# Optimization experiments

Hardware: AMD Instinct MI355X
Metric: run time of the kernel (lower is better)

Reference implementation:

```python
import jax, jax.numpy as jnp
import numpy as np

NUM_HEADS = 32
HEAD_DIM = 128  # 4096 / 32


def setup_inputs() -> dict:
    key = jax.random.key(0)
    k1, k2, k3 = jax.random.split(key, 3)
    B, S, H = 1, 2048, 4096
    hidden_states = jax.random.normal(k1, (B, S, H), dtype=jnp.float32)
    # causal additive mask, broadcast over heads: 0 on/below diagonal, large negative above
    neg = jnp.finfo(jnp.float32).min
    causal = jnp.triu(jnp.full((S, S), neg, dtype=jnp.float32), k=1)
    attention_mask = causal[None, None, :, :]  # [1,1,S,S]
    w_pack = jax.random.normal(k2, (3 * H, H), dtype=jnp.float32) * 0.02
    w_o = jax.random.normal(k3, (H, H), dtype=jnp.float32) * 0.02
    return {"hidden_states": hidden_states, "attention_mask": attention_mask,
            "w_pack": w_pack, "w_o": w_o}


def reference(hidden_states, attention_mask, w_pack, w_o):
    B, S, H = hidden_states.shape
    nh, hd = NUM_HEADS, HEAD_DIM
    # fused QKV projection (Linear, no bias): x @ W^T
    proj = hidden_states @ w_pack.T                      # [B,S,3H]
    q, k, v = jnp.split(proj, 3, axis=-1)
    q = q.reshape(B, S, nh, hd).transpose(0, 2, 1, 3)    # [B,nh,S,hd]
    k = k.reshape(B, S, nh, hd).transpose(0, 2, 1, 3)
    v = v.reshape(B, S, nh, hd).transpose(0, 2, 1, 3)
    scale = 1.0 / jnp.sqrt(jnp.float32(hd))
    attn = jnp.einsum('bhqd,bhkd->bhqk', q, k) * scale   # [B,nh,S,S]
    attn = attn + attention_mask
    attn = jnp.maximum(attn, jnp.finfo(attn.dtype).min)  # clamp like torch.max(..., finfo.min)
    attn = jax.nn.softmax(attn, axis=-1)
    out = jnp.einsum('bhqk,bhkd->bhqd', attn, v)         # [B,nh,S,hd]
    out = out.transpose(0, 2, 1, 3).reshape(B, S, nh * hd)
    return out @ w_o.T                                    # [B,S,H]
```

## Files before the change

kernel.cpp:

```cpp
#include <hip/hip_runtime.h>
#include <stdint.h>

typedef __attribute__((ext_vector_type(8))) short short8;
typedef __attribute__((ext_vector_type(4))) float floatx4;

#define SEQ    2048
#define HID    4096
#define NHEAD  32
#define HDIMV  128
#define PROJN  12288

__device__ __forceinline__ unsigned short f2bf(float f) {
  union { float f; unsigned u; } v; v.f = f;
  unsigned r = (v.u + 0x7fffu + ((v.u >> 16) & 1u)) >> 16;
  return (unsigned short)r;
}

__device__ __forceinline__ void g2l16(const void* g, void* l) {
  __builtin_amdgcn_global_load_lds(
      (const __attribute__((address_space(1))) void*)g,
      (__attribute__((address_space(3))) void*)l, 16, 0, 0);
}

__global__ __launch_bounds__(256) void pack_fp32(const float* __restrict__ src,
                                                 unsigned short* __restrict__ dst, int K,
                                                 int scale_rows, float scale) {
  const int rp = blockIdx.x, kt = blockIdx.y, t = threadIdx.x;
  const long tb = ((long)rp * gridDim.y + kt) * 8192;
#pragma unroll
  for (int j = 0; j < 4; j++) {
    int ch = t + j * 256;
    int r = ch & 127, cc = ch >> 7;
    float sc = (rp * 128 + r < scale_rows) ? scale : 1.0f;
    const float* s = src + (long)(rp * 128 + r) * K + kt * 64 + cc * 8;
    float4 a = *(const float4*)s;
    float4 b = *(const float4*)(s + 4);
    short8 o;
    o[0] = (short)f2bf(a.x * sc); o[1] = (short)f2bf(a.y * sc);
    o[2] = (short)f2bf(a.z * sc); o[3] = (short)f2bf(a.w * sc);
    o[4] = (short)f2bf(b.x * sc); o[5] = (short)f2bf(b.y * sc);
    o[6] = (short)f2bf(b.z * sc); o[7] = (short)f2bf(b.w * sc);
    *(short8*)(dst + tb + ch * 8) = o;
  }
}

template<int OUT_F32>
__global__ __launch_bounds__(256, 4) void gemm_pk(
    const unsigned short* __restrict__ Ap,
    const unsigned short* __restrict__ Bp,
    void* __restrict__ C, int N, int K) {
  __shared__ __align__(16) unsigned short As[8192];
  __shared__ __align__(16) unsigned short Bs[8192];
  const int t = threadIdx.x;
  const int wave = t >> 6, lane = t & 63;
  const int bid = blockIdx.x;
  const int xcd = bid & 7;
  const int li = bid >> 3;
  const int mi = li & 15;
  const int ni = (li >> 4) * 8 + xcd;
  const int KT = K >> 6;
  const unsigned short* at = Ap + (long)mi * KT * 8192 + t * 8;
  const unsigned short* bt = Bp + (long)ni * KT * 8192 + t * 8;
  unsigned short* asl = As + wave * 512;
  unsigned short* bsl = Bs + wave * 512;

  const int mw = (wave >> 1) * 64;
  const int nw = (wave & 1) * 64;
  const int lq = lane & 15, lg = lane >> 4;

  floatx4 zero = {0.f, 0.f, 0.f, 0.f};
  floatx4 acc[4][4];
  for (int i = 0; i < 4; i++)
    for (int j = 0; j < 4; j++) acc[i][j] = zero;

  for (int kt = 0; kt < KT; kt++) {
    __syncthreads();
    const unsigned short* ak = at + (long)kt * 8192;
    const unsigned short* bk = bt + (long)kt * 8192;
#pragma unroll
    for (int j = 0; j < 4; j++) g2l16(ak + j * 2048, asl + j * 2048);
#pragma unroll
    for (int j = 0; j < 4; j++) g2l16(bk + j * 2048, bsl + j * 2048);
    __syncthreads();
#pragma unroll
    for (int kk = 0; kk < 2; kk++) {
      const int ch = (kk * 4 + lg) * 1024;
      short8 af[4], bfr[4];
#pragma unroll
      for (int i = 0; i < 4; i++)
        af[i] = *(const short8*)(As + ch + (mw + i * 16 + lq) * 8);
#pragma unroll
      for (int j = 0; j < 4; j++)
        bfr[j] = *(const short8*)(Bs + ch + (nw + j * 16 + lq) * 8);
#pragma unroll
      for (int i = 0; i < 4; i++)
#pragma unroll
        for (int j = 0; j < 4; j++)
          acc[i][j] = __builtin_amdgcn_mfma_f32_16x16x32_bf16(af[i], bfr[j], acc[i][j], 0, 0, 0);
    }
  }

  const int row0 = mi * 128 + mw + lg * 4;
  const int col0 = ni * 128 + nw + lq;
  if (OUT_F32) {
    float* Cf = (float*)C;
#pragma unroll
    for (int i = 0; i < 4; i++)
#pragma unroll
      for (int j = 0; j < 4; j++)
#pragma unroll
        for (int r = 0; r < 4; r++)
          Cf[(long)(row0 + i * 16 + r) * N + col0 + j * 16] = acc[i][j][r];
  } else {
    unsigned short* Cb = (unsigned short*)C;
#pragma unroll
    for (int i = 0; i < 4; i++)
#pragma unroll
      for (int j = 0; j < 4; j++)
#pragma unroll
        for (int r = 0; r < 4; r++)
          Cb[(long)(row0 + i * 16 + r) * N + col0 + j * 16] = f2bf(acc[i][j][r]);
  }
}

__global__ __launch_bounds__(256, 4) void gemm_qkv(
    const unsigned short* __restrict__ Ap,
    const unsigned short* __restrict__ Bp,
    unsigned short* __restrict__ Qf,
    unsigned short* __restrict__ Kf,
    unsigned short* __restrict__ Vf) {
  __shared__ __align__(16) unsigned short As[8192];
  __shared__ __align__(16) unsigned short Bs[8192];
  const int t = threadIdx.x;
  const int wave = t >> 6, lane = t & 63;
  const int bid = blockIdx.x;
  const int xcd = bid & 7;
  const int li = bid >> 3;
  const int mi = li & 15;
  const int ni = (li >> 4) * 8 + xcd;
  const int KT = HID >> 6;
  const unsigned short* at = Ap + (long)mi * KT * 8192 + t * 8;
  const unsigned short* bt = Bp + (long)ni * KT * 8192 + t * 8;
  unsigned short* asl = As + wave * 512;
  unsigned short* bsl = Bs + wave * 512;

  const int mw = (wave >> 1) * 64;
  const int nw = (wave & 1) * 64;
  const int lq = lane & 15, lg = lane >> 4;

  floatx4 zero = {0.f, 0.f, 0.f, 0.f};
  floatx4 acc[4][4];
  for (int i = 0; i < 4; i++)
    for (int j = 0; j < 4; j++) acc[i][j] = zero;

  for (int kt = 0; kt < KT; kt++) {
    __syncthreads();
    const unsigned short* ak = at + (long)kt * 8192;
    const unsigned short* bk = bt + (long)kt * 8192;
#pragma unroll
    for (int j = 0; j < 4; j++) g2l16(ak + j * 2048, asl + j * 2048);
#pragma unroll
    for (int j = 0; j < 4; j++) g2l16(bk + j * 2048, bsl + j * 2048);
    __syncthreads();
#pragma unroll
    for (int kk = 0; kk < 2; kk++) {
      const int ch = (kk * 4 + lg) * 1024;
      short8 af[4], bfr[4];
#pragma unroll
      for (int i = 0; i < 4; i++)
        af[i] = *(const short8*)(As + ch + (mw + i * 16 + lq) * 8);
#pragma unroll
      for (int j = 0; j < 4; j++)
        bfr[j] = *(const short8*)(Bs + ch + (nw + j * 16 + lq) * 8);
#pragma unroll
      for (int i = 0; i < 4; i++)
#pragma unroll
        for (int j = 0; j < 4; j++)
          acc[i][j] = __builtin_amdgcn_mfma_f32_16x16x32_bf16(af[i], bfr[j], acc[i][j], 0, 0, 0);
    }
  }

  const int sec = ni >> 5;
  const int h = ni & 31;
  unsigned short* dst =
      (sec == 0 ? Qf : (sec == 1 ? Kf : Vf)) + ((long)(h * 16 + mi)) * 16384;
  if (sec < 2) {
#pragma unroll
    for (int i = 0; i < 4; i++)
#pragma unroll
      for (int j = 0; j < 4; j++)
#pragma unroll
        for (int r = 0; r < 4; r++) {
          int row = mw + i * 16 + lg * 4 + r;
          int c = nw + j * 16 + lq;
          dst[((c >> 3) * 128 + row) * 8 + (c & 7)] = f2bf(acc[i][j][r]);
        }
  } else {
#pragma unroll
    for (int i = 0; i < 4; i++)
#pragma unroll
      for (int j = 0; j < 4; j++)
#pragma unroll
        for (int r = 0; r < 4; r++) {
          int s = mw + i * 16 + lg * 4 + r;
          int d = nw + j * 16 + lq;
          dst[((s >> 3) * 128 + d) * 8 + (s & 7)] = f2bf(acc[i][j][r]);
        }
  }
}

__device__ __forceinline__ void stage_tile(const unsigned short* g, unsigned short* lds,
                                           int wave, int lane) {
  const unsigned short* gp = g + wave * 4096 + lane * 8;
  unsigned short* lp = lds + wave * 4096;
#pragma unroll
  for (int j = 0; j < 8; j++) g2l16(gp + j * 512, lp + j * 512);
}

__global__ __launch_bounds__(256, 1) void attn_kernel(
    const unsigned short* __restrict__ Qf,
    const unsigned short* __restrict__ Kf,
    const unsigned short* __restrict__ Vf,
    unsigned short* __restrict__ aop) {
  __shared__ __align__(16) unsigned short Ks[2][16384];
  __shared__ __align__(16) unsigned short Vs[2][16384];
  __shared__ __align__(16) unsigned short Ps[16384];
  const int bx = blockIdx.x;
  const int h = bx & 31;
  const int qt = 15 - (bx >> 5);
  const int t = threadIdx.x, wave = t >> 6, lane = t & 63;
  const int lq = lane & 15, lg = lane >> 4;
  const int wOff = wave * 32;

  const unsigned short* qb = Qf + ((long)(h * 16 + qt)) * 16384;
  short8 qf[2][4];
#pragma unroll
  for (int i = 0; i < 2; i++)
#pragma unroll
    for (int kk = 0; kk < 4; kk++)
      qf[i][kk] = *(const short8*)(qb + ((kk * 4 + lg) * 128 + wOff + i * 16 + lq) * 8);

  float mraw[2][4], lsum[2][4];
  floatx4 zero = {0.f, 0.f, 0.f, 0.f};
  floatx4 o[2][8];
#pragma unroll
  for (int i = 0; i < 2; i++)
#pragma unroll
    for (int r = 0; r < 4; r++) { mraw[i][r] = -INFINITY; lsum[i][r] = 0.f; }
#pragma unroll
  for (int i = 0; i < 2; i++)
#pragma unroll
    for (int j = 0; j < 8; j++) o[i][j] = zero;

  const unsigned short* kb0 = Kf + ((long)h * 16) * 16384;
  const unsigned short* vb0 = Vf + ((long)h * 16) * 16384;
  stage_tile(kb0, Ks[0], wave, lane);
  stage_tile(vb0, Vs[0], wave, lane);

  for (int kv = 0; kv <= qt; kv++) {
    const int cur = kv & 1;
    const bool diag = (kv == qt);
    __syncthreads();
    if (!diag) {
      stage_tile(kb0 + (long)(kv + 1) * 16384, Ks[1 - cur], wave, lane);
      stage_tile(vb0 + (long)(kv + 1) * 16384, Vs[1 - cur], wave, lane);
    }

    floatx4 s[2][8];
#pragma unroll
    for (int i = 0; i < 2; i++)
#pragma unroll
      for (int j = 0; j < 8; j++) s[i][j] = zero;
#pragma unroll
    for (int kk = 0; kk < 4; kk++) {
      short8 bfr[8];
#pragma unroll
      for (int j = 0; j < 8; j++)
        bfr[j] = *(const short8*)(&Ks[cur][((kk * 4 + lg) * 128 + j * 16 + lq) * 8]);
#pragma unroll
      for (int i = 0; i < 2; i++)
#pragma unroll
        for (int j = 0; j < 8; j++)
          s[i][j] = __builtin_amdgcn_mfma_f32_16x16x32_bf16(qf[i][kk], bfr[j], s[i][j], 0, 0, 0);
    }

    if (diag) {
#pragma unroll
      for (int i = 0; i < 2; i++)
#pragma unroll
        for (int r = 0; r < 4; r++) {
          int qrow = qt * 128 + wOff + i * 16 + lg * 4 + r;
#pragma unroll
          for (int j = 0; j < 8; j++)
            if (kv * 128 + j * 16 + lq > qrow) s[i][j][r] = -INFINITY;
        }
    }

    float alpha_[2][4];
#pragma unroll
    for (int i = 0; i < 2; i++) {
#pragma unroll
      for (int r = 0; r < 4; r++) {
        float mx = s[i][0][r];
#pragma unroll
        for (int j = 1; j < 8; j++) mx = fmaxf(mx, s[i][j][r]);
#pragma unroll
        for (int d = 1; d < 16; d <<= 1) mx = fmaxf(mx, __shfl_xor(mx, d, 64));
        float mnew = fmaxf(mraw[i][r], mx);
        float al = exp2f(mraw[i][r] - mnew);
        float ps = 0.f;
#pragma unroll
        for (int j = 0; j < 8; j++) {
          float p = exp2f(s[i][j][r] - mnew);
          s[i][j][r] = p;
          ps += p;
        }
#pragma unroll
        for (int d = 1; d < 16; d <<= 1) ps += __shfl_xor(ps, d, 64);
        lsum[i][r] = lsum[i][r] * al + ps;
        mraw[i][r] = mnew;
        alpha_[i][r] = al;
      }
    }
#pragma unroll
    for (int i = 0; i < 2; i++)
#pragma unroll
      for (int j = 0; j < 8; j++)
#pragma unroll
        for (int r = 0; r < 4; r++) o[i][j][r] *= alpha_[i][r];

#pragma unroll
    for (int i = 0; i < 2; i++)
#pragma unroll
      for (int r = 0; r < 4; r++) {
        int prow = wOff + i * 16 + lg * 4 + r;
#pragma unroll
        for (int j = 0; j < 8; j++)
          Ps[((j * 2 + (lq >> 3)) * 128 + prow) * 8 + (lq & 7)] = f2bf(s[i][j][r]);
      }

#pragma unroll
    for (int kk = 0; kk < 4; kk++) {
      short8 pf[2], vf[8];
#pragma unroll
      for (int i = 0; i < 2; i++)
        pf[i] = *(const short8*)(Ps + ((kk * 4 + lg) * 128 + wOff + i * 16 + lq) * 8);
#pragma unroll
      for (int j = 0; j < 8; j++)
        vf[j] = *(const short8*)(&Vs[cur][((kk * 4 + lg) * 128 + j * 16 + lq) * 8]);
#pragma unroll
      for (int i = 0; i < 2; i++)
#pragma unroll
        for (int j = 0; j < 8; j++)
          o[i][j] = __builtin_amdgcn_mfma_f32_16x16x32_bf16(pf[i], vf[j], o[i][j], 0, 0, 0);
    }
  }

#pragma unroll
  for (int i = 0; i < 2; i++) {
    float inv[4];
#pragma unroll
    for (int r = 0; r < 4; r++) inv[r] = 1.0f / lsum[i][r];
#pragma unroll
    for (int r = 0; r < 4; r++) {
      int prow = wOff + i * 16 + lg * 4 + r;
#pragma unroll
      for (int j = 0; j < 8; j++)
        Ps[((j * 2 + (lq >> 3)) * 128 + prow) * 8 + (lq & 7)] = f2bf(o[i][j][r] * inv[r]);
    }
  }
#pragma unroll
  for (int it = 0; it < 8; it++) {
    int row_loc = it * 4 + (lane >> 4);
    int cc = lane & 15;
    short8 v = *(const short8*)(Ps + (cc * 128 + wOff + row_loc) * 8);
    long tb = ((long)qt * 64 + h * 2 + (cc >> 3)) * 8192;
    *(short8*)(aop + tb + ((cc & 7) * 128 + wOff + row_loc) * 8) = v;
  }
}

extern "C" void kernel_launch(void* const* d_in, const int* in_sizes, int n_in,
                              void* d_out, int out_size, void* d_ws, size_t ws_size,
                              hipStream_t stream) {
  (void)in_sizes; (void)n_in; (void)out_size;
  const float* hs = (const float*)d_in[0];
  const float* wp = (const float*)d_in[2];
  const float* wo = (const float*)d_in[3];
  float* out = (float*)d_out;
  char* ws = (char*)d_ws;

  unsigned short* Ap1 = (unsigned short*)(ws);
  unsigned short* Bp1 = (unsigned short*)(ws + 16777216);
  unsigned short* Bp2 = (unsigned short*)(ws + 117440512);
  unsigned short* Qf  = (unsigned short*)(ws + 150994944);
  unsigned short* Kf  = (unsigned short*)(ws + 167772160);
  unsigned short* Vf  = (unsigned short*)(ws + 184549376);
  unsigned short* aop = (unsigned short*)(ws + 201326592);
  if (ws_size < 218103808) return;

  pack_fp32<<<dim3(16, 64), 256, 0, stream>>>(hs, Ap1, HID, 0, 1.0f);
  pack_fp32<<<dim3(96, 64), 256, 0, stream>>>(wp, Bp1, HID, 4096, 0.12751744154f);
  pack_fp32<<<dim3(32, 64), 256, 0, stream>>>(wo, Bp2, HID, 0, 1.0f);

  gemm_qkv<<<1536, 256, 0, stream>>>(Ap1, Bp1, Qf, Kf, Vf);

  attn_kernel<<<512, 256, 0, stream>>>(Qf, Kf, Vf, aop);

  gemm_pk<1><<<512, 256, 0, stream>>>(aop, Bp2, (void*)out, HID, HID);
}
```

Before: 776.5 us.

## Unify GEMMs into double-buffered 128x256-tile kernel with 8 waves

Replaces the two single-buffered GEMM kernels with one templated kernel. It uses 512 threads, a 128x256 output tile (two packed N tiles per block) and double-buffered LDS, prefetching the next K tile with async global-to-LDS loads while MFMAs run on the current one. It also raises wave priority during the MFMA section and selects the QKV scatter or fp32 output epilogue by template. The aim is to hide global load latency and cut the second barrier per iteration. In exchange, LDS per block grows and occupancy drops to two blocks per CU.

```diff
diff --git a/kernel.cpp b/kernel.cpp
--- a/kernel.cpp
+++ b/kernel.cpp
@@ -44,168 +44,125 @@
   }
 }
 
-template<int OUT_F32>
-__global__ __launch_bounds__(256, 4) void gemm_pk(
+template<int EPI>
+__global__ __launch_bounds__(512, 2) void gemm_db(
     const unsigned short* __restrict__ Ap,
     const unsigned short* __restrict__ Bp,
-    void* __restrict__ C, int N, int K) {
-  __shared__ __align__(16) unsigned short As[8192];
-  __shared__ __align__(16) unsigned short Bs[8192];
+    float* __restrict__ C, int N,
+    unsigned short* __restrict__ Qf,
+    unsigned short* __restrict__ Kf,
+    unsigned short* __restrict__ Vf,
+    int KT) {
+  __shared__ __align__(16) unsigned short As[2][8192];
+  __shared__ __align__(16) unsigned short Bs[2][16384];
   const int t = threadIdx.x;
   const int wave = t >> 6, lane = t & 63;
   const int bid = blockIdx.x;
   const int xcd = bid & 7;
   const int li = bid >> 3;
   const int mi = li & 15;
-  const int ni = (li >> 4) * 8 + xcd;
-  const int KT = K >> 6;
-  const unsigned short* at = Ap + (long)mi * KT * 8192 + t * 8;
-  const unsigned short* bt = Bp + (long)ni * KT * 8192 + t * 8;
-  unsigned short* asl = As + wave * 512;
-  unsigned short* bsl = Bs + wave * 512;
-
-  const int mw = (wave >> 1) * 64;
-  const int nw = (wave & 1) * 64;
+  const int npair = (li >> 4) * 8 + xcd;
+  const unsigned short* at  = Ap + (long)mi * KT * 8192 + t * 8;
+  const unsigned short* bt0 = Bp + (long)(npair * 2) * KT * 8192 + t * 8;
+  const unsigned short* bt1 = Bp + (long)(npair * 2 + 1) * KT * 8192 + t * 8;
+  const int wr = wave >> 2, wc = wave & 3;
+  const int mw = wr * 64;
   const int lq = lane & 15, lg = lane >> 4;
 
   floatx4 zero = {0.f, 0.f, 0.f, 0.f};
   floatx4 acc[4][4];
+#pragma unroll
   for (int i = 0; i < 4; i++)
+#pragma unroll
     for (int j = 0; j < 4; j++) acc[i][j] = zero;
 
+  auto STAGE = [&](int buf, int kt) {
+    const unsigned short* a  = at  + (long)kt * 8192;
+    const unsigned short* b0 = bt0 + (long)kt * 8192;
+    const unsigned short* b1 = bt1 + (long)kt * 8192;
+    unsigned short* al = &As[buf][wave * 512];
+    unsigned short* bl = &Bs[buf][wave * 512];
+    g2l16(a, al);               g2l16(a + 4096, al + 4096);
+    g2l16(b0, bl);              g2l16(b0 + 4096, bl + 4096);
+    g2l16(b1, bl + 8192);       g2l16(b1 + 4096, bl + 12288);
+  };
+
+  STAGE(0, 0);
   for (int kt = 0; kt < KT; kt++) {
-    __syncthreads();
-    const unsigned short* ak = at + (long)kt * 8192;
-    const unsigned short* bk = bt + (long)kt * 8192;
-#pragma unroll
-    for (int j = 0; j < 4; j++) g2l16(ak + j * 2048, asl + j * 2048);
-#pragma unroll
-    for (int j = 0; j < 4; j++) g2l16(bk + j * 2048, bsl + j * 2048);
-    __syncthreads();
+    const int cur = kt & 1;
+    if (kt + 1 < KT) {
+      STAGE(1 - cur, kt + 1);
+      asm volatile("s_waitcnt vmcnt(6)" ::: "memory");
+    } else {
+      asm volatile("s_waitcnt vmcnt(0)" ::: "memory");
+    }
+    __builtin_amdgcn_s_barrier();
+    __builtin_amdgcn_sched_barrier(0);
+    const unsigned short* ab = &As[cur][0];
+    const unsigned short* bb = &Bs[cur][(wc >> 1) * 8192];
+    const int nb = (wc & 1) * 64;
+    __builtin_amdgcn_s_setprio(1);
 #pragma unroll
     for (int kk = 0; kk < 2; kk++) {
-      const int ch = (kk * 4 + lg) * 1024;
+      const int ch = (kk * 4 + lg) * 128;
       short8 af[4], bfr[4];
 #pragma unroll
       for (int i = 0; i < 4; i++)
-        af[i] = *(const short8*)(As + ch + (mw + i * 16 + lq) * 8);
+        af[i] = *(const short8*)(ab + (ch + mw + i * 16 + lq) * 8);
 #pragma unroll
       for (int j = 0; j < 4; j++)
-        bfr[j] = *(const short8*)(Bs + ch + (nw + j * 16 + lq) * 8);
+        bfr[j] = *(const short8*)(bb + (ch + nb + j * 16 + lq) * 8);
 #pragma unroll
       for (int i = 0; i < 4; i++)
 #pragma unroll
         for (int j = 0; j < 4; j++)
           acc[i][j] = __builtin_amdgcn_mfma_f32_16x16x32_bf16(af[i], bfr[j], acc[i][j], 0, 0, 0);
     }
-  }
-
-  const int row0 = mi * 128 + mw + lg * 4;
-  const int col0 = ni * 128 + nw + lq;
-  if (OUT_F32) {
-    float* Cf = (float*)C;
+    __builtin_amdgcn_s_setprio(0);
+    __builtin_amdgcn_sched_barrier(0);
+    __builtin_amdgcn_s_barrier();
+  }
+
+  if (EPI == 0) {
+    const int row0 = mi * 128 + mw + lg * 4;
+    const int col0 = npair * 256 + wc * 64 + lq;
 #pragma unroll
     for (int i = 0; i < 4; i++)
 #pragma unroll
       for (int j = 0; j < 4; j++)
 #pragma unroll
         for (int r = 0; r < 4; r++)
-          Cf[(long)(row0 + i * 16 + r) * N + col0 + j * 16] = acc[i][j][r];
+          C[(long)(row0 + i * 16 + r) * N + col0 + j * 16] = acc[i][j][r];
   } else {
-    unsigned short* Cb = (unsigned short*)C;
-#pragma unroll
-    for (int i = 0; i < 4; i++)
-#pragma unroll
-      for (int j = 0; j < 4; j++)
-#pragma unroll
-        for (int r = 0; r < 4; r++)
-          Cb[(long)(row0 + i * 16 + r) * N + col0 + j * 16] = f2bf(acc[i][j][r]);
-  }
-}
-
-__global__ __launch_bounds__(256, 4) void gemm_qkv(
-    const unsigned short* __restrict__ Ap,
-    const unsigned short* __restrict__ Bp,
-    unsigned short* __restrict__ Qf,
-    unsigned short* __restrict__ Kf,
-    unsigned short* __restrict__ Vf) {
-  __shared__ __align__(16) unsigned short As[8192];
-  __shared__ __align__(16) unsigned short Bs[8192];
-  const int t = threadIdx.x;
-  const int wave = t >> 6, lane = t & 63;
-  const int bid = blockIdx.x;
-  const int xcd = bid & 7;
-  const int li = bid >> 3;
-  const int mi = li & 15;
-  const int ni = (li >> 4) * 8 + xcd;
-  const int KT = HID >> 6;
-  const unsigned short* at = Ap + (long)mi * KT * 8192 + t * 8;
-  const unsigned short* bt = Bp + (long)ni * KT * 8192 + t * 8;
-  unsigned short* asl = As + wave * 512;
-  unsigned short* bsl = Bs + wave * 512;
-
-  const int mw = (wave >> 1) * 64;
-  const int nw = (wave & 1) * 64;
-  const int lq = lane & 15, lg = lane >> 4;
-
-  floatx4 zero = {0.f, 0.f, 0.f, 0.f};
-  floatx4 acc[4][4];
-  for (int i = 0; i < 4; i++)
-    for (int j = 0; j < 4; j++) acc[i][j] = zero;
-
-  for (int kt = 0; kt < KT; kt++) {
-    __syncthreads();
-    const unsigned short* ak = at + (long)kt * 8192;
-    const unsigned short* bk = bt + (long)kt * 8192;
-#pragma unroll
-    for (int j = 0; j < 4; j++) g2l16(ak + j * 2048, asl + j * 2048);
-#pragma unroll
-    for (int j = 0; j < 4; j++) g2l16(bk + j * 2048, bsl + j * 2048);
-    __syncthreads();
-#pragma unroll
-    for (int kk = 0; kk < 2; kk++) {
-      const int ch = (kk * 4 + lg) * 1024;
-      short8 af[4], bfr[4];
+    const int ni = npair * 2 + (wc >> 1);
+    const int sec = ni >> 5;
+    const int h = ni & 31;
+    unsigned short* dst =
+        (sec == 0 ? Qf : (sec == 1 ? Kf : Vf)) + ((long)(h * 16 + mi)) * 16384;
+    const int cb = (wc & 1) * 64;
+    if (sec < 2) {
 #pragma unroll
       for (int i = 0; i < 4; i++)
-        af[i] = *(const short8*)(As + ch + (mw + i * 16 + lq) * 8);
-#pragma unroll
-      for (int j = 0; j < 4; j++)
-        bfr[j] = *(const short8*)(Bs + ch + (nw + j * 16 + lq) * 8);
+#pragma unroll
+        for (int j = 0; j < 4; j++)
+#pragma unroll
+          for (int r = 0; r < 4; r++) {
+            int row = mw + i * 16 + lg * 4 + r;
+            int c = cb + j * 16 + lq;
+            dst[((c >> 3) * 128 + row) * 8 + (c & 7)] = f2bf(acc[i][j][r]);
+          }
+    } else {
 #pragma unroll
       for (int i = 0; i < 4; i++)
 #pragma unroll
         for (int j = 0; j < 4; j++)
-          acc[i][j] = __builtin_amdgcn_mfma_f32_16x16x32_bf16(af[i], bfr[j], acc[i][j], 0, 0, 0);
-    }
-  }
-
-  const int sec = ni >> 5;
-  const int h = ni & 31;
-  unsigned short* dst =
-      (sec == 0 ? Qf : (sec == 1 ? Kf : Vf)) + ((long)(h * 16 + mi)) * 16384;
-  if (sec < 2) {
-#pragma unroll
-    for (int i = 0; i < 4; i++)
-#pragma unroll
-      for (int j = 0; j < 4; j++)
-#pragma unroll
-        for (int r = 0; r < 4; r++) {
-          int row = mw + i * 16 + lg * 4 + r;
-          int c = nw + j * 16 + lq;
-          dst[((c >> 3) * 128 + row) * 8 + (c & 7)] = f2bf(acc[i][j][r]);
-        }
-  } else {
-#pragma unroll
-    for (int i = 0; i < 4; i++)
-#pragma unroll
-      for (int j = 0; j < 4; j++)
-#pragma unroll
-        for (int r = 0; r < 4; r++) {
-          int s = mw + i * 16 + lg * 4 + r;
-          int d = nw + j * 16 + lq;
-          dst[((s >> 3) * 128 + d) * 8 + (s & 7)] = f2bf(acc[i][j][r]);
-        }
+#pragma unroll
+          for (int r = 0; r < 4; r++) {
+            int s = mw + i * 16 + lg * 4 + r;
+            int d = cb + j * 16 + lq;
+            dst[((s >> 3) * 128 + d) * 8 + (s & 7)] = f2bf(acc[i][j][r]);
+          }
+    }
   }
 }
 
@@ -402,9 +359,9 @@
   pack_fp32<<<dim3(96, 64), 256, 0, stream>>>(wp, Bp1, HID, 4096, 0.12751744154f);
   pack_fp32<<<dim3(32, 64), 256, 0, stream>>>(wo, Bp2, HID, 0, 1.0f);
 
-  gemm_qkv<<<1536, 256, 0, stream>>>(Ap1, Bp1, Qf, Kf, Vf);
+  gemm_db<1><<<768, 512, 0, stream>>>(Ap1, Bp1, nullptr, PROJN, Qf, Kf, Vf, HID >> 6);
 
   attn_kernel<<<512, 256, 0, stream>>>(Qf, Kf, Vf, aop);
 
-  gemm_pk<1><<<512, 256, 0, stream>>>(aop, Bp2, (void*)out, HID, HID);
-}
+  gemm_db<0><<<256, 512, 0, stream>>>(aop, Bp2, out, HID, nullptr, nullptr, nullptr, HID >> 6);
+}
```

After: 893.5 us. 15.1% more time.
